# Performance work log

Hardware: AMD Instinct MI355X
Metric: run time of the kernel (lower is better)

The kernel has to match this reference:

```python
import jax, jax.numpy as jnp
import numpy as np

B, N, C = 4, 1024, 1024
H, TD, MULT = 16, 256, 4
HD = C // H
MAX_LEN = 1024
EPS = 1e-5


def _layer_norm(x, g, b):
    m = jnp.mean(x, axis=-1, keepdims=True)
    v = jnp.mean((x - m) ** 2, axis=-1, keepdims=True)
    return (x - m) / jnp.sqrt(v + EPS) * g + b


def _skew(x):
    # x: [B,H,N,M] -> pad left on last dim, reshape, drop first row -> [B,H,N,M]
    b, h, n, m = x.shape
    x = jnp.pad(x, ((0, 0), (0, 0), (0, 0), (1, 0)))
    x = x.reshape(b, h, m + 1, n)
    return x[:, :, 1:, :]


def setup_inputs() -> dict:
    key = jax.random.key(0)
    ks = jax.random.split(key, 16)
    s = 0.02
    return {
        "x": jax.random.normal(ks[0], (B, N, C), jnp.float32),
        "t": jax.random.normal(ks[1], (B, TD), jnp.float32),
        "ln1_g": jnp.ones((C,), jnp.float32),
        "ln1_b": jnp.zeros((C,), jnp.float32),
        "qkv_w": jax.random.normal(ks[2], (C, 3 * C), jnp.float32) * s,
        "qkv_b": jnp.zeros((3 * C,), jnp.float32),
        "time_w": jax.random.normal(ks[3], (TD, 3 * C), jnp.float32) * s,
        "time_b": jnp.zeros((3 * C,), jnp.float32),
        "out_w": jax.random.normal(ks[4], (C, C), jnp.float32) * s,
        "out_b": jnp.zeros((C,), jnp.float32),
        "Er": jax.random.normal(ks[5], (MAX_LEN, HD), jnp.float32) * s,
        "ln2_g": jnp.ones((C,), jnp.float32),
        "ln2_b": jnp.zeros((C,), jnp.float32),
        "ff1_w": jax.random.normal(ks[6], (C, MULT * C), jnp.float32) * s,
        "ff1_b": jnp.zeros((MULT * C,), jnp.float32),
        "ff2_w": jax.random.normal(ks[7], (MULT * C, C), jnp.float32) * s,
        "ff2_b": jnp.zeros((C,), jnp.float32),
    }


def reference(x, t, ln1_g, ln1_b, qkv_w, qkv_b, time_w, time_b, out_w, out_b,
              Er, ln2_g, ln2_b, ff1_w, ff1_b, ff2_w, ff2_b):
    # ---- attention branch ----
    xn = _layer_norm(x, ln1_g, ln1_b)
    qkv = (xn @ qkv_w + qkv_b).reshape(B, N, 3, H, HD).transpose(2, 0, 3, 1, 4)
    q, k, v = qkv[0], qkv[1], qkv[2]  # [B,H,N,HD]
    tqkv = (t @ time_w + time_b).reshape(B, 1, 3, H, HD).transpose(2, 0, 3, 1, 4)
    q = q + tqkv[0]
    k = k + tqkv[1]
    v = v + tqkv[2]
    Er_n = Er[MAX_LEN - N:]  # [N,HD]
    rel = jnp.einsum('bhnd,md->bhnm', q, Er_n)
    rel = _skew(rel)
    scale = HD ** -0.5
    attn = jnp.einsum('bhnd,bhmd->bhnm', q, k) * scale + rel
    attn = jax.nn.softmax(attn, axis=-1)
    out = jnp.einsum('bhnm,bhmd->bhnd', attn, v)
    out = out.transpose(0, 2, 1, 3).reshape(B, N, C)
    x = x + (out @ out_w + out_b)
    # ---- FFN branch ----
    h = _layer_norm(x, ln2_g, ln2_b)
    h = jax.nn.gelu(h @ ff1_w + ff1_b, approximate=False)
    x = x + (h @ ff2_w + ff2_b)
    return x
```

## Files before the change

### kernel.cpp

```cpp
#include <hip/hip_runtime.h>
#include <hip/hip_bf16.h>

typedef __attribute__((ext_vector_type(8))) short short8;
typedef __attribute__((ext_vector_type(4))) float f32x4;
typedef __attribute__((ext_vector_type(16))) float f32x16;

#define DEV __device__ __forceinline__

DEV float bf2f(ushort u){ union { float f; unsigned int i; } x; x.i = ((unsigned int)u)<<16; return x.f; }
DEV ushort f2bf(float f){ union { float fl; unsigned int i; } x; x.fl = f; unsigned int r = x.i + 0x7fffu + ((x.i>>16)&1u); return (ushort)(r>>16); }

DEV void gl2lds16(const ushort* g, ushort* l){
  __builtin_amdgcn_global_load_lds((const __attribute__((address_space(1))) void*)g,
                                   (__attribute__((address_space(3))) void*)l, 16, 0, 0);
}
DEV f32x16 mfma32(short8 a, short8 b, f32x16 c){
  return __builtin_amdgcn_mfma_f32_32x32x16_bf16(a, b, c, 0, 0, 0);
}
DEV uint cvtpk(float lo, float hi){
  uint r; asm("v_cvt_pk_bf16_f32 %0, %1, %2" : "=v"(r) : "v"(lo), "v"(hi));
  return r;
}
DEV uint q8(float v){
  float c = fminf(fmaxf(v, -127.f), 127.f);
  return ((uint)(int)rintf(c)) & 255u;
}

__global__ void cvt_f2b(const float* __restrict__ in, ushort* __restrict__ out, int n){
  int i = blockIdx.x*blockDim.x + threadIdx.x;
  int stride = gridDim.x*blockDim.x;
  for (; i < n; i += stride) out[i] = f2bf(in[i]);
}

__global__ __launch_bounds__(256) void wt_cvt(const float* __restrict__ in, ushort* __restrict__ out,
                                              int K, int N, int ldk){
  const int n0 = blockIdx.x*64, k0 = blockIdx.y*64;
  __shared__ float T[64][65];
  const int tid = threadIdx.x;
  const int r = tid>>4, c = (tid&15)*4;
  #pragma unroll
  for (int p=0;p<4;p++){
    float4 v = *(const float4*)&in[(size_t)(k0 + p*16 + r)*N + n0 + c];
    T[p*16+r][c+0]=v.x; T[p*16+r][c+1]=v.y; T[p*16+r][c+2]=v.z; T[p*16+r][c+3]=v.w;
  }
  __syncthreads();
  #pragma unroll
  for (int p=0;p<4;p++){
    int n = p*16 + r;
    ushort u0 = f2bf(T[c+0][n]), u1 = f2bf(T[c+1][n]), u2 = f2bf(T[c+2][n]), u3 = f2bf(T[c+3][n]);
    ushort4 u = make_ushort4(u0,u1,u2,u3);
    *(ushort4*)&out[(size_t)(n0+n)*ldk + k0 + c] = u;
  }
}

__global__ __launch_bounds__(256) void vt_k(const ushort* __restrict__ qkv, ushort* __restrict__ vt){
  const int bh = blockIdx.y; const int b = bh>>4, h = bh&15;
  const int n0 = blockIdx.x*64;
  __shared__ ushort T[64][66];
  const int tid = threadIdx.x;
  const int r = tid>>3, c8 = (tid&7)*8;
  #pragma unroll
  for (int p=0;p<2;p++){
    int row = p*32 + r;
    short8 v = *(const short8*)&qkv[(size_t)(b*1024 + n0 + row)*3200 + 2048 + h*64 + c8];
    #pragma unroll
    for (int i=0;i<8;i++) T[row][c8+i] = ((ushort*)&v)[i];
  }
  __syncthreads();
  #pragma unroll
  for (int p=0;p<2;p++){
    int d = p*32 + r;
    union { ushort u[8]; short8 v; } o;
    #pragma unroll
    for (int i=0;i<8;i++) o.u[i] = T[c8+i][d];
    *(short8*)&vt[(size_t)(bh*64 + d)*1152 + n0 + c8] = o.v;
  }
}

__global__ __launch_bounds__(256) void ln_rows(const float* __restrict__ in,
                                               const float* __restrict__ g,
                                               const float* __restrict__ bta,
                                               ushort* __restrict__ out, int ldo){
  int row = blockIdx.x; int tid = threadIdx.x;
  const float* x = in + (size_t)row*1024;
  float v[4]; float s = 0.f;
  #pragma unroll
  for (int i=0;i<4;i++){ v[i] = x[tid + 256*i]; s += v[i]; }
  __shared__ float rbuf[256];
  rbuf[tid] = s; __syncthreads();
  for (int off=128; off>0; off>>=1){ if (tid<off) rbuf[tid]+=rbuf[tid+off]; __syncthreads(); }
  float mean = rbuf[0] * (1.f/1024.f);
  __syncthreads();
  float s2 = 0.f;
  #pragma unroll
  for (int i=0;i<4;i++){ float d=v[i]-mean; s2 += d*d; }
  rbuf[tid] = s2; __syncthreads();
  for (int off=128; off>0; off>>=1){ if (tid<off) rbuf[tid]+=rbuf[tid+off]; __syncthreads(); }
  float var = rbuf[0] * (1.f/1024.f);
  float rstd = rsqrtf(var + 1e-5f);
  #pragma unroll
  for (int i=0;i<4;i++){ int c = tid+256*i; out[(size_t)row*ldo+c] = f2bf((v[i]-mean)*rstd*g[c]+bta[c]); }
}

__global__ __launch_bounds__(256) void tq_gemm2(const float* __restrict__ t, const float* __restrict__ tw,
                                                const float* __restrict__ tb, float* __restrict__ tq){
  const int tid = threadIdx.x;
  const int j = blockIdx.x*64 + (tid & 63);
  const int sl = tid >> 6;
  float acc[4] = {0.f,0.f,0.f,0.f};
  for (int k = sl*64; k < sl*64+64; ++k){
    float wv = tw[(size_t)k*3072 + j];
    #pragma unroll
    for (int b=0;b<4;b++) acc[b] = fmaf(t[b*256+k], wv, acc[b]);
  }
  __shared__ float red[4][4][64];
  #pragma unroll
  for (int b=0;b<4;b++) red[sl][b][tid&63] = acc[b];
  __syncthreads();
  if (sl == 0){
    #pragma unroll
    for (int b=0;b<4;b++)
      tq[b*3072 + j] = red[0][b][tid&63] + red[1][b][tid&63] + red[2][b][tid&63] + red[3][b][tid&63] + tb[j];
  }
}

template<int EPI, int TN>
__global__ __launch_bounds__(256) void gemm4(
    const ushort* __restrict__ A, const ushort* __restrict__ Bt,
    const float* __restrict__ bias, const float* __restrict__ extra,
    ushort* __restrict__ outb, float* __restrict__ outf,
    int K, int lda, int ldb, int ldo, int lde, int nbx)
{
  constexpr int NJ = TN/32;
  __shared__ __align__(16) ushort Al[2][128*32];
  __shared__ __align__(16) ushort Bl[2][TN*32];
  const int nwg = gridDim.x, cpx = nwg >> 3;
  const int bid = blockIdx.x;
  const int swz = (bid & 7)*cpx + (bid >> 3);
  const int m0 = (swz / nbx)*128, n0 = (swz % nbx)*TN;
  const int tid = threadIdx.x, lane = tid & 63, wid = tid >> 6;
  const int wm = (wid&1)*64, wn = (wid>>1)*(TN/2);
  const int l15 = lane&15, l4 = lane>>4;
  f32x4 acc[4][NJ];
  #pragma unroll
  for (int i=0;i<4;i++)
    #pragma unroll
    for (int jx=0;jx<NJ;jx++){ acc[i][jx][0]=0.f; acc[i][jx][1]=0.f; acc[i][jx][2]=0.f; acc[i][jx][3]=0.f; }
  const ushort* a0p = A + (size_t)(m0 + (tid>>2))*lda + (tid&3)*8;
  const ushort* a1p = A + (size_t)(m0 + 64 + (tid>>2))*lda + (tid&3)*8;
  const ushort* b0p = Bt + (size_t)(n0 + (tid>>2))*ldb + (tid&3)*8;
  const ushort* b1p = nullptr;
  if constexpr (TN==128) b1p = Bt + (size_t)(n0 + 64 + (tid>>2))*ldb + (tid&3)*8;
  const int lsl = tid*8, lsh = (tid+256)*8;

  gl2lds16(a0p, &Al[0][lsl]);
  gl2lds16(a1p, &Al[0][lsh]);
  gl2lds16(b0p, &Bl[0][lsl]);
  if constexpr (TN==128) gl2lds16(b1p, &Bl[0][lsh]);
  __syncthreads();

  const int nk = K >> 5;
  for (int it=0; it<nk; ++it){
    const int cur = it & 1;
    ushort* Ac = Al[cur];  ushort* Bc = Bl[cur];
    if (it+1 < nk){
      const int k1 = (it+1) << 5;
      gl2lds16(a0p + k1, &Al[cur^1][lsl]);
      gl2lds16(a1p + k1, &Al[cur^1][lsh]);
      gl2lds16(b0p + k1, &Bl[cur^1][lsl]);
      if constexpr (TN==128) gl2lds16(b1p + k1, &Bl[cur^1][lsh]);
    }
    short8 af[4], bfr[NJ];
    #pragma unroll
    for (int mi=0;mi<4;mi++) af[mi]  = *(const short8*)&Ac[(wm + mi*16 + l15)*32 + l4*8];
    #pragma unroll
    for (int nj=0;nj<NJ;nj++) bfr[nj] = *(const short8*)&Bc[(wn + nj*16 + l15)*32 + l4*8];
    #pragma unroll
    for (int mi=0;mi<4;mi++)
      #pragma unroll
      for (int nj=0;nj<NJ;nj++)
        acc[mi][nj] = __builtin_amdgcn_mfma_f32_16x16x32_bf16(af[mi], bfr[nj], acc[mi][nj], 0,0,0);
    __syncthreads();
  }
  #pragma unroll
  for (int mi=0;mi<4;mi++)
    #pragma unroll
    for (int nj=0;nj<NJ;nj++)
      #pragma unroll
      for (int j=0;j<4;j++){
        int row = m0 + wm + mi*16 + l4*4 + j;
        int col = n0 + wn + nj*16 + l15;
        float v = acc[mi][nj][j] + bias[col];
        if constexpr (EPI==0){ v += extra[(size_t)(row>>10)*lde + col]; outb[(size_t)row*ldo+col] = f2bf(v); }
        else if constexpr (EPI==1){ v += extra[(size_t)row*lde + col]; outf[(size_t)row*ldo+col] = v; }
        else { v = 0.5f*v*(1.f+erff(v*0.70710678118f)); outb[(size_t)row*ldo+col] = f2bf(v); }
      }
}

__global__ __launch_bounds__(256) void relskew8_v3(
    const ushort* __restrict__ qkv, const ushort* __restrict__ Er,
    signed char* __restrict__ srel)
{
  const int bid0 = blockIdx.x;
  const int swz = (bid0 & 7)*256 + (bid0 >> 3);
  const int bh = swz >> 5, b = bh >> 4, h = bh & 15;
  const int r0 = (swz & 31)*32;
  const int tid = threadIdx.x, w = tid >> 6, lane = tid & 63;
  const int l31 = lane & 31, hi = lane >> 5;

  __shared__ signed char T8[33*1040];
  signed char* srb = srel + (size_t)bh*1024*1040;

  if (tid < 33){
    int tgt = r0 - 1 + tid;
    int c = tgt + 1;
    if (tgt >= 0 && c <= 1023) T8[tid*1040 + c] = 0;
  }

  const ushort* Qp = qkv + (size_t)b*1024*3200 + h*64;
  const int r = r0 + l31;
  short8 qf0 = *(const short8*)(Qp + (size_t)r*3200 +      hi*8);
  short8 qf1 = *(const short8*)(Qp + (size_t)r*3200 + 16 + hi*8);
  short8 qf2 = *(const short8*)(Qp + (size_t)r*3200 + 32 + hi*8);
  short8 qf3 = *(const short8*)(Qp + (size_t)r*3200 + 48 + hi*8);

  const float ESC = 92.332481f;
  for (int t=0; t<8; ++t){
    const int e0 = w*256 + t*32;
    const ushort* ep = Er + (size_t)(e0 + l31)*64 + hi*8;
    short8 ea0 = *(const short8*)(ep);
    short8 ea1 = *(const short8*)(ep + 16);
    short8 ea2 = *(const short8*)(ep + 32);
    short8 ea3 = *(const short8*)(ep + 48);
    f32x16 acc = {};
    acc = mfma32(ea0, qf0, acc);
    acc = mfma32(ea1, qf1, acc);
    acc = mfma32(ea2, qf2, acc);
    acc = mfma32(ea3, qf3, acc);
    #pragma unroll
    for (int q=0;q<4;q++)
      #pragma unroll
      for (int j=0;j<4;j++){
        int e = e0 + 8*q + 4*hi + j;
        signed char v = (signed char)(int)q8(acc[4*q+j]*ESC);
        bool below = (e + r) >= 1023;
        int i = below ? (l31 + 1) : l31;
        int c = e + r + (below ? -1023 : 1);
        T8[i*1040 + c] = v;
      }
  }
  __syncthreads();

  const int c4 = tid*4;
  #pragma unroll 4
  for (int i=0; i<33; ++i){
    int tgt = r0 - 1 + i;
    if (tgt < 0) continue;
    int lo = (i==0) ? (r0+1) : 0;
    int hh = (i==32) ? min(r0+32, 1023) : 1023;
    if (c4 >= lo && c4+3 <= hh){
      *(uint*)(srb + (size_t)tgt*1040 + c4) = *(const uint*)&T8[i*1040 + c4];
    } else if (c4 <= hh && c4+3 >= lo){
      #pragma unroll
      for (int k2=0;k2<4;k2++){
        int c = c4 + k2;
        if (c >= lo && c <= hh) srb[(size_t)tgt*1040 + c] = T8[i*1040 + c];
      }
    }
  }
}

__global__ __launch_bounds__(256) void attn9s(
    const ushort* __restrict__ qkv, const signed char* __restrict__ srel,
    const ushort* __restrict__ Vt, float* __restrict__ part)
{
  const int bid0 = blockIdx.x;
  const int swz = (bid0 & 7)*128 + (bid0 >> 3);
  const int bh = swz >> 4, b = bh >> 4, h = bh & 15;
  const int rblk = ((swz >> 1) & 7)*128;
  const int kvh = swz & 1;
  const int tid = threadIdx.x, w = tid >> 6, lane = tid & 63;
  const int l31 = lane & 31, hi = lane >> 5;
  const int r = rblk + w*32 + l31;
  const ushort* Qp = qkv + (size_t)b*1024*3200 + h*64;
  const ushort* Kp = Qp + 1024;
  const ushort* Vp = Vt + (size_t)bh*64*1152;
  const signed char* Bp = srel + (size_t)bh*1024*1040 + (size_t)r*1040 + hi*4;

  short8 qf0 = *(const short8*)(Qp + (size_t)r*3200 +      hi*8);
  short8 qf1 = *(const short8*)(Qp + (size_t)r*3200 + 16 + hi*8);
  short8 qf2 = *(const short8*)(Qp + (size_t)r*3200 + 32 + hi*8);
  short8 qf3 = *(const short8*)(Qp + (size_t)r*3200 + 48 + hi*8);

  f32x16 O0 = {}, O1 = {};
  float lsum = 0.f;

  const int t0 = kvh*16, tend = t0 + 15;
  short8 kA0 = *(const short8*)(Kp + (size_t)(t0*32 + l31)*3200 +      hi*8);
  short8 kA1 = *(const short8*)(Kp + (size_t)(t0*32 + l31)*3200 + 16 + hi*8);
  short8 kA2 = *(const short8*)(Kp + (size_t)(t0*32 + l31)*3200 + 32 + hi*8);
  short8 kA3 = *(const short8*)(Kp + (size_t)(t0*32 + l31)*3200 + 48 + hi*8);
  short8 kB0, kB1, kB2, kB3;

  auto step = [&](short8& ka0, short8& ka1, short8& ka2, short8& ka3,
                  short8& kn0, short8& kn1, short8& kn2, short8& kn3, int t){
    const int c0 = t*32;
    if (t < tend){
      const ushort* kp = Kp + (size_t)(c0 + 32 + l31)*3200 + hi*8;
      kn0 = *(const short8*)(kp);
      kn1 = *(const short8*)(kp + 16);
      kn2 = *(const short8*)(kp + 32);
      kn3 = *(const short8*)(kp + 48);
    }
    uint bw[4];
    #pragma unroll
    for (int rq=0;rq<4;rq++) bw[rq] = *(const uint*)(Bp + c0 + rq*8);
    short8 v00 = *(const short8*)(Vp + (size_t)l31*1152      + c0 +      hi*8);
    short8 v01 = *(const short8*)(Vp + (size_t)l31*1152      + c0 + 16 + hi*8);
    short8 v10 = *(const short8*)(Vp + (size_t)(32+l31)*1152 + c0 +      hi*8);
    short8 v11 = *(const short8*)(Vp + (size_t)(32+l31)*1152 + c0 + 16 + hi*8);
    f32x16 S = {};
    __builtin_amdgcn_s_setprio(1);
    S = mfma32(ka0, qf0, S);
    S = mfma32(ka1, qf1, S);
    S = mfma32(ka2, qf2, S);
    S = mfma32(ka3, qf3, S);
    __builtin_amdgcn_s_setprio(0);
    float p[16];
    float s0=0.f, s1=0.f, s2=0.f, s3=0.f;
    #pragma unroll
    for (int rq=0;rq<4;rq++)
      #pragma unroll
      for (int j=0;j<4;j++){
        float bias = (float)(signed char)((bw[rq] >> (8*j)) & 255u) * 0.015625f;
        float pv = __builtin_amdgcn_exp2f(fmaf(S[rq*4+j], 0.18033688f, bias));
        p[rq*4+j] = pv;
        if (j==0) s0 += pv; else if (j==1) s1 += pv; else if (j==2) s2 += pv; else s3 += pv;
      }
    lsum += (s0+s1)+(s2+s3);
    uint W00=cvtpk(p[0],p[1]),   W01=cvtpk(p[2],p[3]);
    uint W10=cvtpk(p[4],p[5]),   W11=cvtpk(p[6],p[7]);
    uint W20=cvtpk(p[8],p[9]),   W21=cvtpk(p[10],p[11]);
    uint W30=cvtpk(p[12],p[13]), W31=cvtpk(p[14],p[15]);
    uint x00 = (uint)__shfl_xor((int)(hi? W00 : W10), 32, 64);
    uint x01 = (uint)__shfl_xor((int)(hi? W01 : W11), 32, 64);
    uint x10 = (uint)__shfl_xor((int)(hi? W20 : W30), 32, 64);
    uint x11 = (uint)__shfl_xor((int)(hi? W21 : W31), 32, 64);
    union { uint u[4]; short8 v; } pf0, pf1;
    pf0.u[0] = hi ? x00 : W00;  pf0.u[1] = hi ? x01 : W01;
    pf0.u[2] = hi ? W10 : x00;  pf0.u[3] = hi ? W11 : x01;
    pf1.u[0] = hi ? x10 : W20;  pf1.u[1] = hi ? x11 : W21;
    pf1.u[2] = hi ? W30 : x10;  pf1.u[3] = hi ? W31 : x11;
    __builtin_amdgcn_s_setprio(1);
    O0 = mfma32(v00, pf0.v, O0);
    O0 = mfma32(v01, pf1.v, O0);
    O1 = mfma32(v10, pf0.v, O1);
    O1 = mfma32(v11, pf1.v, O1);
    __builtin_amdgcn_s_setprio(0);
  };
  for (int t=t0; t<t0+16; t+=2){
    step(kA0,kA1,kA2,kA3, kB0,kB1,kB2,kB3, t);
    step(kB0,kB1,kB2,kB3, kA0,kA1,kA2,kA3, t+1);
  }
  float lrow = lsum + __shfl_xor(lsum, 32, 64);

  float* pp = part + ((size_t)kvh*65536 + (size_t)bh*1024 + r)*68;
  #pragma unroll
  for (int rq=0;rq<4;rq++)
    #pragma unroll
    for (int s=0;s<2;s++){
      int reg = rq*4 + s*2;
      int d = rq*8 + hi*4 + s*2;
      *(float2*)(pp + d)      = make_float2(O0[reg], O0[reg+1]);
      *(float2*)(pp + 32 + d) = make_float2(O1[reg], O1[reg+1]);
    }
  if (hi == 0) pp[64] = lrow;
}

__global__ __launch_bounds__(256) void attn_merge(const float* __restrict__ part,
                                                  ushort* __restrict__ out){
  const int row = blockIdx.x*32 + (threadIdx.x>>3);
  const int dseg = (threadIdx.x&7)*8;
  const int bh = row>>10, rr = row&1023, b = bh>>4, h = bh&15;
  const float* p0 = part + (size_t)row*68;
  const float* p1 = part + ((size_t)65536 + row)*68;
  float inv = 1.f/(p0[64] + p1[64]);
  float4 a0 = *(const float4*)(p0 + dseg), a1 = *(const float4*)(p0 + dseg + 4);
  float4 b0 = *(const float4*)(p1 + dseg), b1 = *(const float4*)(p1 + dseg + 4);
  union { uint u[4]; short8 v; } ov;
  ov.u[0] = cvtpk((a0.x+b0.x)*inv, (a0.y+b0.y)*inv);
  ov.u[1] = cvtpk((a0.z+b0.z)*inv, (a0.w+b0.w)*inv);
  ov.u[2] = cvtpk((a1.x+b1.x)*inv, (a1.y+b1.y)*inv);
  ov.u[3] = cvtpk((a1.z+b1.z)*inv, (a1.w+b1.w)*inv);
  *(short8*)&out[((size_t)(b*1024 + rr))*1152 + h*64 + dseg] = ov.v;
}

extern "C" void kernel_launch(void* const* d_in, const int* in_sizes, int n_in,
                              void* d_out, int out_size, void* d_ws, size_t ws_size,
                              hipStream_t stream)
{
  const float* x    = (const float*)d_in[0];
  const float* t    = (const float*)d_in[1];
  const float* ln1g = (const float*)d_in[2];
  const float* ln1b = (const float*)d_in[3];
  const float* qkvw = (const float*)d_in[4];
  const float* qkvb = (const float*)d_in[5];
  const float* timew= (const float*)d_in[6];
  const float* timeb= (const float*)d_in[7];
  const float* outw = (const float*)d_in[8];
  const float* outbv= (const float*)d_in[9];
  const float* Er   = (const float*)d_in[10];
  const float* ln2g = (const float*)d_in[11];
  const float* ln2b = (const float*)d_in[12];
  const float* ff1w = (const float*)d_in[13];
  const float* ff1b = (const float*)d_in[14];
  const float* ff2w = (const float*)d_in[15];
  const float* ff2b = (const float*)d_in[16];
  float* o = (float*)d_out;

  char* ws = (char*)d_ws;
  ushort* qkvw_t = (ushort*)(ws);
  ushort* outw_t = (ushort*)(ws + 7077888);
  ushort* ff1w_t = (ushort*)(ws + 9437184);
  ushort* ff2w_t = (ushort*)(ws + 18874368);
  ushort* er_b   = (ushort*)(ws + 27525120);
  float*  tq     = (float*) (ws + 27656192);
  ushort* bufA   = (ushort*)(ws + 27705344);
  ushort* vt     = (ushort*)(ws + 37142528);
  ushort* bufB   = (ushort*)(ws + 46579712);
  signed char* srel8 = (signed char*)(ws + 81182720);
  float* part    = (float*)(ws + 150994944);

  wt_cvt<<<dim3(48,16),256,0,stream>>>(qkvw, qkvw_t, 1024, 3072, 1152);
  wt_cvt<<<dim3(16,16),256,0,stream>>>(outw, outw_t, 1024, 1024, 1152);
  wt_cvt<<<dim3(64,16),256,0,stream>>>(ff1w, ff1w_t, 1024, 4096, 1152);
  wt_cvt<<<dim3(16,64),256,0,stream>>>(ff2w, ff2w_t, 4096, 1024, 4224);
  cvt_f2b<<<256,256,0,stream>>>(Er, er_b, 65536);

  ln_rows<<<4096,256,0,stream>>>(x, ln1g, ln1b, bufA, 1152);
  tq_gemm2<<<48,256,0,stream>>>(t, timew, timeb, tq);
  gemm4<0,128><<<768,256,0,stream>>>(bufA, qkvw_t, qkvb, tq, bufB, nullptr,
                                     1024, 1152, 1152, 3200, 3072, 24);
  vt_k<<<dim3(16,64),256,0,stream>>>(bufB, vt);
  relskew8_v3<<<2048,256,0,stream>>>(bufB, er_b, srel8);
  attn9s<<<1024,256,0,stream>>>(bufB, srel8, vt, part);
  attn_merge<<<2048,256,0,stream>>>(part, bufA);
  gemm4<1,64><<<512,256,0,stream>>>(bufA, outw_t, outbv, x, nullptr, o,
                                    1024, 1152, 1152, 1024, 1024, 16);
  ln_rows<<<4096,256,0,stream>>>(o, ln2g, ln2b, bufA, 1152);
  gemm4<2,128><<<1024,256,0,stream>>>(bufA, ff1w_t, ff1b, nullptr, bufB, nullptr,
                                      1024, 1152, 1152, 4224, 0, 32);
  gemm4<1,64><<<512,256,0,stream>>>(bufB, ff2w_t, ff2b, o, nullptr, o,
                                    4096, 4224, 4224, 1024, 1024, 16);
}
```

Before: 391.5 us.

## Triple-buffer GEMM LDS pipeline and drop attention KV split-merge

The GEMM kernel moves from a double-buffered to a three-stage LDS ring. Loads are issued two k-steps ahead, with an explicit vmcnt wait and one barrier per iteration, so global-to-LDS latency is better hidden. Separately, the attention kernel no longer splits the KV range in half and writes fp32 partials for a separate merge kernel. Each block now processes all 32 KV tiles and writes normalized bf16 output directly, removing the partial buffer traffic and one launch at the cost of half as many attention blocks (less parallelism).

After: 370.1 us. 1.06x faster.

```diff
diff --git a/kernel.cpp b/kernel.cpp
--- a/kernel.cpp
+++ b/kernel.cpp
@@ -125,15 +125,15 @@
 }
 
 template<int EPI, int TN>
-__global__ __launch_bounds__(256) void gemm4(
+__global__ __launch_bounds__(256) void gemm5(
     const ushort* __restrict__ A, const ushort* __restrict__ Bt,
     const float* __restrict__ bias, const float* __restrict__ extra,
     ushort* __restrict__ outb, float* __restrict__ outf,
     int K, int lda, int ldb, int ldo, int lde, int nbx)
 {
   constexpr int NJ = TN/32;
-  __shared__ __align__(16) ushort Al[2][128*32];
-  __shared__ __align__(16) ushort Bl[2][TN*32];
+  __shared__ __align__(16) ushort Al[3][128*32];
+  __shared__ __align__(16) ushort Bl[3][TN*32];
   const int nwg = gridDim.x, cpx = nwg >> 3;
   const int bid = blockIdx.x;
   const int swz = (bid & 7)*cpx + (bid >> 3);
@@ -153,23 +153,29 @@
   if constexpr (TN==128) b1p = Bt + (size_t)(n0 + 64 + (tid>>2))*ldb + (tid&3)*8;
   const int lsl = tid*8, lsh = (tid+256)*8;
 
-  gl2lds16(a0p, &Al[0][lsl]);
-  gl2lds16(a1p, &Al[0][lsh]);
-  gl2lds16(b0p, &Bl[0][lsl]);
-  if constexpr (TN==128) gl2lds16(b1p, &Bl[0][lsh]);
-  __syncthreads();
+  auto stage = [&](int s, int k1){
+    gl2lds16(a0p + k1, &Al[s][lsl]);
+    gl2lds16(a1p + k1, &Al[s][lsh]);
+    gl2lds16(b0p + k1, &Bl[s][lsl]);
+    if constexpr (TN==128) gl2lds16(b1p + k1, &Bl[s][lsh]);
+  };
 
   const int nk = K >> 5;
+  stage(0, 0);
+  stage(1, 32);
+  int s = 0;
   for (int it=0; it<nk; ++it){
-    const int cur = it & 1;
-    ushort* Ac = Al[cur];  ushort* Bc = Bl[cur];
-    if (it+1 < nk){
-      const int k1 = (it+1) << 5;
-      gl2lds16(a0p + k1, &Al[cur^1][lsl]);
-      gl2lds16(a1p + k1, &Al[cur^1][lsh]);
-      gl2lds16(b0p + k1, &Bl[cur^1][lsl]);
-      if constexpr (TN==128) gl2lds16(b1p + k1, &Bl[cur^1][lsh]);
+    if constexpr (TN==128)
+      asm volatile("s_waitcnt vmcnt(4) lgkmcnt(0)" ::: "memory");
+    else
+      asm volatile("s_waitcnt vmcnt(3) lgkmcnt(0)" ::: "memory");
+    __builtin_amdgcn_sched_barrier(0);
+    __builtin_amdgcn_s_barrier();
+    if (it+2 < nk){
+      int s2 = s + 2; if (s2 >= 3) s2 -= 3;
+      stage(s2, (it+2) << 5);
     }
+    ushort* Ac = Al[s];  ushort* Bc = Bl[s];
     short8 af[4], bfr[NJ];
     #pragma unroll
     for (int mi=0;mi<4;mi++) af[mi]  = *(const short8*)&Ac[(wm + mi*16 + l15)*32 + l4*8];
@@ -180,7 +186,7 @@
       #pragma unroll
       for (int nj=0;nj<NJ;nj++)
         acc[mi][nj] = __builtin_amdgcn_mfma_f32_16x16x32_bf16(af[mi], bfr[nj], acc[mi][nj], 0,0,0);
-    __syncthreads();
+    if (++s >= 3) s = 0;
   }
   #pragma unroll
   for (int mi=0;mi<4;mi++)
@@ -270,15 +276,14 @@
   }
 }
 
-__global__ __launch_bounds__(256) void attn9s(
+__global__ __launch_bounds__(256) void attn9(
     const ushort* __restrict__ qkv, const signed char* __restrict__ srel,
-    const ushort* __restrict__ Vt, float* __restrict__ part)
+    const ushort* __restrict__ Vt, ushort* __restrict__ out)
 {
   const int bid0 = blockIdx.x;
-  const int swz = (bid0 & 7)*128 + (bid0 >> 3);
-  const int bh = swz >> 4, b = bh >> 4, h = bh & 15;
-  const int rblk = ((swz >> 1) & 7)*128;
-  const int kvh = swz & 1;
+  const int swz = (bid0 & 7)*64 + (bid0 >> 3);
+  const int bh = swz >> 3, b = bh >> 4, h = bh & 15;
+  const int rblk = (swz & 7)*128;
   const int tid = threadIdx.x, w = tid >> 6, lane = tid & 63;
   const int l31 = lane & 31, hi = lane >> 5;
   const int r = rblk + w*32 + l31;
@@ -295,17 +300,16 @@
   f32x16 O0 = {}, O1 = {};
   float lsum = 0.f;
 
-  const int t0 = kvh*16, tend = t0 + 15;
-  short8 kA0 = *(const short8*)(Kp + (size_t)(t0*32 + l31)*3200 +      hi*8);
-  short8 kA1 = *(const short8*)(Kp + (size_t)(t0*32 + l31)*3200 + 16 + hi*8);
-  short8 kA2 = *(const short8*)(Kp + (size_t)(t0*32 + l31)*3200 + 32 + hi*8);
-  short8 kA3 = *(const short8*)(Kp + (size_t)(t0*32 + l31)*3200 + 48 + hi*8);
+  short8 kA0 = *(const short8*)(Kp + (size_t)l31*3200 +      hi*8);
+  short8 kA1 = *(const short8*)(Kp + (size_t)l31*3200 + 16 + hi*8);
+  short8 kA2 = *(const short8*)(Kp + (size_t)l31*3200 + 32 + hi*8);
+  short8 kA3 = *(const short8*)(Kp + (size_t)l31*3200 + 48 + hi*8);
   short8 kB0, kB1, kB2, kB3;
 
   auto step = [&](short8& ka0, short8& ka1, short8& ka2, short8& ka3,
                   short8& kn0, short8& kn1, short8& kn2, short8& kn3, int t){
     const int c0 = t*32;
-    if (t < tend){
+    if (t < 31){
       const ushort* kp = Kp + (size_t)(c0 + 32 + l31)*3200 + hi*8;
       kn0 = *(const short8*)(kp);
       kn1 = *(const short8*)(kp + 16);
@@ -358,41 +362,23 @@
     O1 = mfma32(v11, pf1.v, O1);
     __builtin_amdgcn_s_setprio(0);
   };
-  for (int t=t0; t<t0+16; t+=2){
+  for (int t=0;t<32;t+=2){
     step(kA0,kA1,kA2,kA3, kB0,kB1,kB2,kB3, t);
     step(kB0,kB1,kB2,kB3, kA0,kA1,kA2,kA3, t+1);
   }
-  float lrow = lsum + __shfl_xor(lsum, 32, 64);
-
-  float* pp = part + ((size_t)kvh*65536 + (size_t)bh*1024 + r)*68;
+  float inv = 1.f/(lsum + __shfl_xor(lsum, 32, 64));
+  ushort* op = out + ((size_t)(b*1024 + r))*1152 + h*64;
   #pragma unroll
   for (int rq=0;rq<4;rq++)
     #pragma unroll
     for (int s=0;s<2;s++){
       int reg = rq*4 + s*2;
+      uint w0 = cvtpk(O0[reg]*inv, O0[reg+1]*inv);
+      uint w1 = cvtpk(O1[reg]*inv, O1[reg+1]*inv);
       int d = rq*8 + hi*4 + s*2;
-      *(float2*)(pp + d)      = make_float2(O0[reg], O0[reg+1]);
-      *(float2*)(pp + 32 + d) = make_float2(O1[reg], O1[reg+1]);
+      *(uint*)(op + d) = w0;
+      *(uint*)(op + 32 + d) = w1;
     }
-  if (hi == 0) pp[64] = lrow;
-}
-
-__global__ __launch_bounds__(256) void attn_merge(const float* __restrict__ part,
-                                                  ushort* __restrict__ out){
-  const int row = blockIdx.x*32 + (threadIdx.x>>3);
-  const int dseg = (threadIdx.x&7)*8;
-  const int bh = row>>10, rr = row&1023, b = bh>>4, h = bh&15;
-  const float* p0 = part + (size_t)row*68;
-  const float* p1 = part + ((size_t)65536 + row)*68;
-  float inv = 1.f/(p0[64] + p1[64]);
-  float4 a0 = *(const float4*)(p0 + dseg), a1 = *(const float4*)(p0 + dseg + 4);
-  float4 b0 = *(const float4*)(p1 + dseg), b1 = *(const float4*)(p1 + dseg + 4);
-  union { uint u[4]; short8 v; } ov;
-  ov.u[0] = cvtpk((a0.x+b0.x)*inv, (a0.y+b0.y)*inv);
-  ov.u[1] = cvtpk((a0.z+b0.z)*inv, (a0.w+b0.w)*inv);
-  ov.u[2] = cvtpk((a1.x+b1.x)*inv, (a1.y+b1.y)*inv);
-  ov.u[3] = cvtpk((a1.z+b1.z)*inv, (a1.w+b1.w)*inv);
-  *(short8*)&out[((size_t)(b*1024 + rr))*1152 + h*64 + dseg] = ov.v;
 }
 
 extern "C" void kernel_launch(void* const* d_in, const int* in_sizes, int n_in,
@@ -429,7 +415,6 @@
   ushort* vt     = (ushort*)(ws + 37142528);
   ushort* bufB   = (ushort*)(ws + 46579712);
   signed char* srel8 = (signed char*)(ws + 81182720);
-  float* part    = (float*)(ws + 150994944);
 
   wt_cvt<<<dim3(48,16),256,0,stream>>>(qkvw, qkvw_t, 1024, 3072, 1152);
   wt_cvt<<<dim3(16,16),256,0,stream>>>(outw, outw_t, 1024, 1024, 1152);
@@ -439,17 +424,16 @@
 
   ln_rows<<<4096,256,0,stream>>>(x, ln1g, ln1b, bufA, 1152);
   tq_gemm2<<<48,256,0,stream>>>(t, timew, timeb, tq);
-  gemm4<0,128><<<768,256,0,stream>>>(bufA, qkvw_t, qkvb, tq, bufB, nullptr,
+  gemm5<0,128><<<768,256,0,stream>>>(bufA, qkvw_t, qkvb, tq, bufB, nullptr,
                                      1024, 1152, 1152, 3200, 3072, 24);
   vt_k<<<dim3(16,64),256,0,stream>>>(bufB, vt);
   relskew8_v3<<<2048,256,0,stream>>>(bufB, er_b, srel8);
-  attn9s<<<1024,256,0,stream>>>(bufB, srel8, vt, part);
-  attn_merge<<<2048,256,0,stream>>>(part, bufA);
-  gemm4<1,64><<<512,256,0,stream>>>(bufA, outw_t, outbv, x, nullptr, o,
+  attn9<<<512,256,0,stream>>>(bufB, srel8, vt, bufA);
+  gemm5<1,64><<<512,256,0,stream>>>(bufA, outw_t, outbv, x, nullptr, o,
                                     1024, 1152, 1152, 1024, 1024, 16);
   ln_rows<<<4096,256,0,stream>>>(o, ln2g, ln2b, bufA, 1152);
-  gemm4<2,128><<<1024,256,0,stream>>>(bufA, ff1w_t, ff1b, nullptr, bufB, nullptr,
+  gemm5<2,128><<<1024,256,0,stream>>>(bufA, ff1w_t, ff1b, nullptr, bufB, nullptr,
                                       1024, 1152, 1152, 4224, 0, 32);
-  gemm4<1,64><<<512,256,0,stream>>>(bufB, ff2w_t, ff2b, o, nullptr, o,
+  gemm5<1,64><<<512,256,0,stream>>>(bufB, ff2w_t, ff2b, o, nullptr, o,
                                     4096, 4224, 4224, 1024, 1024, 16);
 }
```
